# Kernel optimization log

Hardware: AMD Instinct MI355X
Metric: run time of the kernel (lower is better)

The kernel has to match this reference:

```python
import jax, jax.numpy as jnp
import numpy as np

N, E, EE = 1024, 32768, 262144
C_S, C_Z, C_G, H, R = 384, 128, 16, 4, 64
EPS = 1e-8


def _rbf(d, D_count=R, D_min=0.0, D_max=20.0):
    # gvp-style radial basis: exp(-((d - mu)/sigma)^2), mu in linspace(D_min, D_max)
    mu = jnp.linspace(D_min, D_max, D_count, dtype=d.dtype)
    sigma = (D_max - D_min) / D_count
    return jnp.exp(-(((d[..., None] - mu) / sigma) ** 2))


def _layernorm(x, g, b, eps=1e-5):
    m = jnp.mean(x, axis=-1, keepdims=True)
    v = jnp.var(x, axis=-1, keepdims=True)
    return (x - m) * jax.lax.rsqrt(v + eps) * g + b


def setup_inputs() -> dict:
    key = jax.random.key(0)
    ks = jax.random.split(key, 32)
    s = 0.02
    inp = {
        'node_features': jax.random.normal(ks[0], (N, C_S), jnp.float32),
        'node_trans': jax.random.normal(ks[1], (N, 3), jnp.float32) * 10.0,
        'edge_features': jax.random.normal(ks[2], (E, C_Z), jnp.float32),
        'edge_index': jax.random.randint(ks[3], (2, E), 0, N),
        'edge_edge_index': jax.random.randint(ks[4], (2, EE), 0, E),
        # layer norm
        'ln_g': jnp.ones((C_Z,), jnp.float32),
        'ln_b': jnp.zeros((C_Z,), jnp.float32),
        # node_left / node_right
        'W_nl': jax.random.normal(ks[5], (C_S, C_G), jnp.float32) * s,
        'b_nl': jnp.zeros((C_G,), jnp.float32),
        'W_nr': jax.random.normal(ks[6], (C_S, C_G), jnp.float32) * s,
        'b_nr': jnp.zeros((C_G,), jnp.float32),
        # bias_gate: (c_gate_s^2 -> c_z)
        'W_bg': jax.random.normal(ks[7], (C_G * C_G, C_Z), jnp.float32) * s,
        'b_bg': jnp.zeros((C_Z,), jnp.float32),
        # dist_bias: (num_rbf -> c_z)
        'W_db': jax.random.normal(ks[8], (R, C_Z), jnp.float32) * s,
        'b_db': jnp.zeros((C_Z,), jnp.float32),
        # to_bias: (c_z -> num_heads), no bias
        'W_tb': jax.random.normal(ks[9], (C_Z, H), jnp.float32) * s,
        # q / kv
        'W_q': jax.random.normal(ks[10], (C_Z, C_Z), jnp.float32) * s,
        'b_q': jnp.zeros((C_Z,), jnp.float32),
        'W_kv': jax.random.normal(ks[11], (C_Z, 2 * C_Z), jnp.float32) * s,
        'b_kv': jnp.zeros((2 * C_Z,), jnp.float32),
        # out gate + out proj
        'W_og': jax.random.normal(ks[12], (C_Z, C_Z), jnp.float32) * s,
        'b_og': jnp.zeros((C_Z,), jnp.float32),
        'W_out': jax.random.normal(ks[13], (C_Z, C_Z), jnp.float32) * s,
        'b_out': jnp.zeros((C_Z,), jnp.float32),
    }
    return inp


def reference(node_features, node_trans, edge_features, edge_index, edge_edge_index,
              ln_g, ln_b, W_nl, b_nl, W_nr, b_nr, W_bg, b_bg, W_db, b_db, W_tb,
              W_q, b_q, W_kv, b_kv, W_og, b_og, W_out, b_out):
    d = C_Z // H
    ee0, ee1 = edge_edge_index[0], edge_edge_index[1]
    # node indices of the two triangle corner nodes for each edge-edge pair
    n1 = edge_index[0, ee1]  # [EE]
    n2 = edge_index[0, ee0]  # [EE]

    ef = _layernorm(edge_features, ln_g, ln_b)  # [E, c_z]

    nl = node_features @ W_nl + b_nl  # [N, c_g]
    nr = node_features @ W_nr + b_nr
    # outer product gate features per edge-edge pair
    e3 = jnp.einsum('bi,bj->bij', nl[n1], nr[n2]).reshape(-1, C_G * C_G)  # [EE, c_g^2]
    gate = e3 @ W_bg + b_bg  # [EE, c_z]

    dist = jnp.linalg.norm(node_trans[n1] - node_trans[n2] + EPS, axis=-1)  # [EE]
    dist_bias = _rbf(dist) @ W_db + b_db  # [EE, c_z]
    bias = (jax.nn.sigmoid(gate) * dist_bias) @ W_tb  # [EE, H]

    q = (ef @ W_q + b_q).reshape(E, H, d)
    kv = ef @ W_kv + b_kv
    k = kv[:, :C_Z].reshape(E, H, d)
    v = kv[:, C_Z:].reshape(E, H, d)

    attn = jnp.einsum('bhi,bhi->bh', q[ee1], k[ee0]) * (1.0 / np.sqrt(C_Z)) + bias  # [EE, H]

    # segment softmax over target edge ee1
    seg_max = jax.ops.segment_max(attn, ee1, num_segments=E)  # [E, H]
    p = jnp.exp(attn - seg_max[ee1])
    seg_sum = jax.ops.segment_sum(p, ee1, num_segments=E)
    p = p / (seg_sum[ee1] + 1e-16)

    upd = jax.ops.segment_sum(v[ee0] * p[..., None], ee1, num_segments=E)  # [E, H, d]
    upd = upd.reshape(E, C_Z)
    upd = upd * jax.nn.sigmoid(ef @ W_og + b_og)
    return upd @ W_out + b_out
```

## Files before the change

kernel.cpp:

```cpp
#include <hip/hip_runtime.h>
#include <math.h>

#define NN 1024
#define NE 32768
#define NEE 262144
#define CS 384
#define CZ 128
#define CG 16
#define NH 4
#define NR 64

typedef __attribute__((ext_vector_type(8))) short short8v;
typedef __attribute__((ext_vector_type(4))) float f32x4;
typedef unsigned short ushort_t;

__device__ __forceinline__ float sigmoidf_(float x) { return 1.0f / (1.0f + __expf(-x)); }

__device__ __forceinline__ ushort_t f2bf(float x) {
    union { float f; unsigned u; } v; v.f = x;
    unsigned r = v.u + 0x7fff + ((v.u >> 16) & 1);
    return (ushort_t)(r >> 16);
}
__device__ __forceinline__ float bf2f(ushort_t x) {
    union { unsigned u; float f; } v; v.u = ((unsigned)x) << 16;
    return v.f;
}

__global__ void node_proj_kernel(const float* __restrict__ nf,
                                 const float* __restrict__ Wl, const float* __restrict__ bl,
                                 const float* __restrict__ Wr, const float* __restrict__ br,
                                 ushort_t* __restrict__ nl16, float* __restrict__ nr) {
    int wave = threadIdx.x >> 6, lane = threadIdx.x & 63;
    int n = blockIdx.x * 4 + wave;
    if (lane >= 32) return;
    bool isl = lane < 16;
    int o = isl ? lane : lane - 16;
    const float* W = isl ? Wl : Wr;
    float acc = isl ? bl[o] : br[o];
    const float* x = nf + n * CS;
    for (int k = 0; k < CS; ++k) acc += x[k] * W[k * 16 + o];
    if (isl) nl16[n * 16 + o] = f2bf(acc);
    else     nr[n * 16 + o] = acc;
}

__global__ void build_Tt_kernel(const float* __restrict__ nr, const float* __restrict__ Wbg,
                                ushort_t* __restrict__ Tbf) {
    int n = blockIdx.x;
    int t = threadIdx.x;
    int c = t & 127, i0 = t >> 7;
    __shared__ float nrs[16];
    if (t < 16) nrs[t] = nr[n * 16 + t];
    __syncthreads();
    for (int i = i0; i < 16; i += 2) {
        float acc = 0.f;
#pragma unroll
        for (int j = 0; j < 16; ++j) acc += nrs[j] * Wbg[(i * 16 + j) * 128 + c];
        Tbf[n * 2048 + c * 16 + i] = f2bf(acc);
    }
}

__global__ void ln_kernel(const float* __restrict__ x, const float* __restrict__ g,
                          const float* __restrict__ b, ushort_t* __restrict__ ef) {
    int wave = threadIdx.x >> 6, lane = threadIdx.x & 63;
    int e = blockIdx.x * 4 + wave;
    int c0 = lane, c1 = lane + 64;
    float x0 = x[e * 128 + c0], x1 = x[e * 128 + c1];
    float s = x0 + x1;
#pragma unroll
    for (int m = 1; m < 64; m <<= 1) s += __shfl_xor(s, m);
    float mean = s * (1.f / 128.f);
    float d0 = x0 - mean, d1 = x1 - mean;
    float v = d0 * d0 + d1 * d1;
#pragma unroll
    for (int m = 1; m < 64; m <<= 1) v += __shfl_xor(v, m);
    v *= (1.f / 128.f);
    float inv = rsqrtf(v + 1e-5f);
    ef[e * 128 + c0] = f2bf(d0 * inv * g[c0] + b[c0]);
    ef[e * 128 + c1] = f2bf(d1 * inv * g[c1] + b[c1]);
}

__global__ void prep_w_kernel(const float* __restrict__ Wq, const float* __restrict__ bq,
                              const float* __restrict__ Wkv, const float* __restrict__ bkv,
                              const float* __restrict__ Wog, const float* __restrict__ bog,
                              const float* __restrict__ Wdb, const float* __restrict__ Wout,
                              ushort_t* __restrict__ WcatT, float* __restrict__ bcat,
                              ushort_t* __restrict__ WdbT, ushort_t* __restrict__ WoutT) {
    int idx = blockIdx.x * 256 + threadIdx.x;
    int col = idx >> 7, k = idx & 127;
    float w;
    if (col < 128) w = Wq[k * 128 + col];
    else if (col < 256) w = Wog[k * 128 + (col - 128)];
    else if (col < 384) w = Wkv[k * 256 + (col - 256)];
    else w = Wkv[k * 256 + 128 + (col - 384)];
    WcatT[idx] = f2bf(w);
    if (idx < 512) {
        float bb;
        if (idx < 128) bb = bq[idx];
        else if (idx < 256) bb = bog[idx - 128];
        else if (idx < 384) bb = bkv[idx - 256];
        else bb = bkv[idx - 384 + 128];
        bcat[idx] = bb;
    }
    if (idx < 128 * 64) {
        int c = idx >> 6, r = idx & 63;
        WdbT[idx] = f2bf(Wdb[r * 128 + c]);
    }
    if (idx < 128 * 128) {
        int c = idx >> 7, kk = idx & 127;
        WoutT[idx] = f2bf(Wout[kk * 128 + c]);
    }
}

__global__ void __launch_bounds__(256) mfma_gemm_proj(const ushort_t* __restrict__ Abf,
                                                      const ushort_t* __restrict__ Bt,
                                                      const float* __restrict__ bias,
                                                      ushort_t* __restrict__ qog,
                                                      ushort_t* __restrict__ kvo) {
    __shared__ ushort_t As[128][136];
    __shared__ ushort_t Bs[64][136];
    int t = threadIdx.x;
    int row0 = blockIdx.y * 128;
    int n0 = blockIdx.x * 64;
#pragma unroll
    for (int u = 0; u < 8; ++u) {
        int idx = t + u * 256;
        int r = idx >> 4, seg = idx & 15;
        *(short8v*)&As[r][seg * 8] = *(const short8v*)&Abf[(size_t)(row0 + r) * 128 + seg * 8];
    }
#pragma unroll
    for (int u = 0; u < 4; ++u) {
        int idx = t + u * 256;
        int r = idx >> 4, seg = idx & 15;
        *(short8v*)&Bs[r][seg * 8] = *(const short8v*)&Bt[(size_t)(n0 + r) * 128 + seg * 8];
    }
    __syncthreads();
    int lane = t & 63, w = t >> 6;
    int wr = (w >> 1) * 64, wc = (w & 1) * 32;
    int fr = lane & 15, fk = (lane >> 4) * 8;
    f32x4 acc[4][2] = {};
#pragma unroll
    for (int kk = 0; kk < 4; ++kk) {
        short8v a[4], b[2];
#pragma unroll
        for (int m = 0; m < 4; ++m) a[m] = *(const short8v*)&As[wr + m * 16 + fr][kk * 32 + fk];
#pragma unroll
        for (int n = 0; n < 2; ++n) b[n] = *(const short8v*)&Bs[wc + n * 16 + fr][kk * 32 + fk];
#pragma unroll
        for (int m = 0; m < 4; ++m)
#pragma unroll
            for (int n = 0; n < 2; ++n)
                acc[m][n] = __builtin_amdgcn_mfma_f32_16x16x32_bf16(a[m], b[n], acc[m][n], 0, 0, 0);
    }
    __syncthreads();
    ushort_t (*stage)[72] = (ushort_t(*)[72])&As[0][0];
    int orow = (lane >> 4) * 4;
#pragma unroll
    for (int m = 0; m < 4; ++m)
#pragma unroll
        for (int n = 0; n < 2; ++n) {
            int col = wc + n * 16 + fr;
            float bv = bias[n0 + col];
#pragma unroll
            for (int j = 0; j < 4; ++j)
                stage[wr + m * 16 + orow + j][col] = f2bf(acc[m][n][j] + bv);
        }
    __syncthreads();
    ushort_t* basep; int cbase;
    if (n0 < 256) { basep = qog; cbase = n0; } else { basep = kvo; cbase = n0 - 256; }
#pragma unroll
    for (int u = 0; u < 4; ++u) {
        int idx = t + u * 256;
        int r = idx >> 3, seg = idx & 7;
        *(short8v*)&basep[(size_t)(row0 + r) * 256 + cbase + seg * 8] = *(const short8v*)&stage[r][seg * 8];
    }
}

__global__ void __launch_bounds__(256) mfma_gemm_out(const float* __restrict__ Af,
                                                     const ushort_t* __restrict__ Bt,
                                                     const float* __restrict__ bias,
                                                     float* __restrict__ out) {
    __shared__ ushort_t As[128][136];
    __shared__ ushort_t Bs[64][136];
    int t = threadIdx.x;
    int row0 = blockIdx.y * 128;
    int n0 = blockIdx.x * 64;
#pragma unroll
    for (int u = 0; u < 8; ++u) {
        int idx = t + u * 256;
        int r = idx >> 4, seg = idx & 15;
        float4 f0 = *(const float4*)&Af[(size_t)(row0 + r) * 128 + seg * 8];
        float4 f1 = *(const float4*)&Af[(size_t)(row0 + r) * 128 + seg * 8 + 4];
        short8v pk;
        pk[0] = (short)f2bf(f0.x); pk[1] = (short)f2bf(f0.y);
        pk[2] = (short)f2bf(f0.z); pk[3] = (short)f2bf(f0.w);
        pk[4] = (short)f2bf(f1.x); pk[5] = (short)f2bf(f1.y);
        pk[6] = (short)f2bf(f1.z); pk[7] = (short)f2bf(f1.w);
        *(short8v*)&As[r][seg * 8] = pk;
    }
#pragma unroll
    for (int u = 0; u < 4; ++u) {
        int idx = t + u * 256;
        int r = idx >> 4, seg = idx & 15;
        *(short8v*)&Bs[r][seg * 8] = *(const short8v*)&Bt[(size_t)(n0 + r) * 128 + seg * 8];
    }
    __syncthreads();
    int lane = t & 63, w = t >> 6;
    int wr = (w >> 1) * 64, wc = (w & 1) * 32;
    int fr = lane & 15, fk = (lane >> 4) * 8;
    f32x4 acc[4][2] = {};
#pragma unroll
    for (int kk = 0; kk < 4; ++kk) {
        short8v a[4], b[2];
#pragma unroll
        for (int m = 0; m < 4; ++m) a[m] = *(const short8v*)&As[wr + m * 16 + fr][kk * 32 + fk];
#pragma unroll
        for (int n = 0; n < 2; ++n) b[n] = *(const short8v*)&Bs[wc + n * 16 + fr][kk * 32 + fk];
#pragma unroll
        for (int m = 0; m < 4; ++m)
#pragma unroll
            for (int n = 0; n < 2; ++n)
                acc[m][n] = __builtin_amdgcn_mfma_f32_16x16x32_bf16(a[m], b[n], acc[m][n], 0, 0, 0);
    }
    __syncthreads();
    float (*stage)[68] = (float(*)[68])&As[0][0];
    int orow = (lane >> 4) * 4;
#pragma unroll
    for (int m = 0; m < 4; ++m)
#pragma unroll
        for (int n = 0; n < 2; ++n) {
            int col = wc + n * 16 + fr;
            float bv = bias[n0 + col];
#pragma unroll
            for (int j = 0; j < 4; ++j)
                stage[wr + m * 16 + orow + j][col] = acc[m][n][j] + bv;
        }
    __syncthreads();
#pragma unroll
    for (int u = 0; u < 8; ++u) {
        int idx = t + u * 256;
        int r = idx >> 4, c4 = idx & 15;
        *(float4*)&out[(size_t)(row0 + r) * 128 + n0 + c4 * 4] = *(const float4*)&stage[r][c4 * 4];
    }
}

__global__ void hist_kernel(const int* __restrict__ eei, const int* __restrict__ ei,
                            int* __restrict__ cnt, int* __restrict__ cnt2) {
    int p = blockIdx.x * 256 + threadIdx.x;
    int e0 = eei[p], e1 = eei[NEE + p];
    atomicAdd(&cnt[e1], 1);
    atomicAdd(&cnt2[ei[e0]], 1);
}

__global__ void scan_kernel(const int* __restrict__ cnt, int* __restrict__ offs,
                            int* __restrict__ cursor) {
    __shared__ int part[1024];
    int t = threadIdx.x;
    int loc[32];
    int s = 0;
#pragma unroll
    for (int j = 0; j < 32; ++j) { loc[j] = cnt[t * 32 + j]; s += loc[j]; }
    part[t] = s;
    __syncthreads();
    for (int d = 1; d < 1024; d <<= 1) {
        int add = (t >= d) ? part[t - d] : 0;
        __syncthreads();
        part[t] += add;
        __syncthreads();
    }
    int excl = (t == 0) ? 0 : part[t - 1];
#pragma unroll
    for (int j = 0; j < 32; ++j) {
        offs[t * 32 + j] = excl;
        cursor[t * 32 + j] = excl;
        excl += loc[j];
    }
    if (t == 1023) offs[NE] = excl;
}

__global__ void scan2_kernel(const int* __restrict__ cnt2, int* __restrict__ offs2,
                             int* __restrict__ cursor2) {
    __shared__ int part[256];
    int t = threadIdx.x;
    int loc[4];
    int s = 0;
#pragma unroll
    for (int j = 0; j < 4; ++j) { loc[j] = cnt2[t * 4 + j]; s += loc[j]; }
    part[t] = s;
    __syncthreads();
    for (int d = 1; d < 256; d <<= 1) {
        int add = (t >= d) ? part[t - d] : 0;
        __syncthreads();
        part[t] += add;
        __syncthreads();
    }
    int excl = (t == 0) ? 0 : part[t - 1];
#pragma unroll
    for (int j = 0; j < 4; ++j) {
        offs2[t * 4 + j] = excl;
        cursor2[t * 4 + j] = excl;
        excl += loc[j];
    }
    if (t == 255) offs2[1024] = excl;
}

__global__ void scatter_both_kernel(const int* __restrict__ eei, const int* __restrict__ ei,
                                    const float* __restrict__ ntr,
                                    int* __restrict__ cursor, int* __restrict__ e0rank,
                                    int* __restrict__ cursor2, int* __restrict__ n1rank,
                                    float* __restrict__ drank, int* __restrict__ x2to1) {
    int p = blockIdx.x * 256 + threadIdx.x;
    int e0 = eei[p], e1 = eei[NEE + p];
    int pos = atomicAdd(&cursor[e1], 1);
    e0rank[pos] = e0;
    int n1 = ei[e1], n2 = ei[e0];
    int pos2 = atomicAdd(&cursor2[n2], 1);
    n1rank[pos2] = n1;
    x2to1[pos2] = pos;
    float dx = ntr[n1 * 3 + 0] - ntr[n2 * 3 + 0] + 1e-8f;
    float dy = ntr[n1 * 3 + 1] - ntr[n2 * 3 + 1] + 1e-8f;
    float dz = ntr[n1 * 3 + 2] - ntr[n2 * 3 + 2] + 1e-8f;
    drank[pos2] = sqrtf(dx * dx + dy * dy + dz * dz);
}

__global__ void __launch_bounds__(256) bias_kernel(
    const int* __restrict__ offs2, const int* __restrict__ n1rank,
    const float* __restrict__ drank, const int* __restrict__ x2to1,
    const ushort_t* __restrict__ nl16, const ushort_t* __restrict__ Tbf,
    const ushort_t* __restrict__ WdbT,
    const float* __restrict__ bbg, const float* __restrict__ bdb,
    const float* __restrict__ Wtb, float* __restrict__ bias_cs) {
    __shared__ ushort_t Tt[128 * 24];
    __shared__ ushort_t Wd[128 * 72];
    int t = threadIdx.x;
    int n2 = blockIdx.x;
    {
        const ushort_t* src = Tbf + n2 * 2048;
        int c = t >> 1, hh = t & 1;
        *(int4*)&Tt[c * 24 + hh * 8] = *(const int4*)&src[c * 16 + hh * 8];
    }
#pragma unroll
    for (int u = 0; u < 4; ++u) {
        int idx = t + u * 256;
        int c = idx >> 3, seg = idx & 7;
        *(int4*)&Wd[c * 72 + seg * 8] = *(const int4*)&WdbT[c * 64 + seg * 8];
    }
    __syncthreads();

    int lane = t & 63, w = t >> 6;
    int cl = lane & 15, g = lane >> 4;
    float wtb[8][4], bdbl[8], bbgl[8];
#pragma unroll
    for (int nb = 0; nb < 8; ++nb) {
        int c = nb * 16 + cl;
        float4 wt = *(const float4*)&Wtb[c * 4];
        wtb[nb][0] = wt.x; wtb[nb][1] = wt.y; wtb[nb][2] = wt.z; wtb[nb][3] = wt.w;
        bdbl[nb] = bdb[c];
        bbgl[nb] = bbg[c];
    }
    int bstart = offs2[n2], bend = offs2[n2 + 1];
    const float MU = 20.0f / 63.0f;
    f32x4 zero4 = {0.f, 0.f, 0.f, 0.f};

    for (int base = bstart + w * 16; base < bend; base += 64) {
        int idx = base + cl;
        int ip = (idx < bend) ? idx : (bend - 1);
        int n1 = n1rank[ip];
        float d = drank[ip];
        short8v aNL = {0, 0, 0, 0, 0, 0, 0, 0};
        if (g < 2) aNL = *(const short8v*)&nl16[n1 * 16 + g * 8];
        short8v ea, eb;
#pragma unroll
        for (int j = 0; j < 8; ++j) {
            float r = (float)(g * 8 + j);
            float t0 = (d - r * MU) * 3.2f;
            float t1 = (d - (r + 32.0f) * MU) * 3.2f;
            ea[j] = (short)f2bf(__expf(-t0 * t0));
            eb[j] = (short)f2bf(__expf(-t1 * t1));
        }
        f32x4 G[8], D[8];
#pragma unroll
        for (int nb = 0; nb < 8; ++nb) {
            short8v bT = {0, 0, 0, 0, 0, 0, 0, 0};
            if (g < 2) bT = *(const short8v*)&Tt[(nb * 16 + cl) * 24 + g * 8];
            G[nb] = __builtin_amdgcn_mfma_f32_16x16x32_bf16(aNL, bT, zero4, 0, 0, 0);
        }
#pragma unroll
        for (int nb = 0; nb < 8; ++nb) {
            short8v bW0 = *(const short8v*)&Wd[(nb * 16 + cl) * 72 + g * 8];
            short8v bW1 = *(const short8v*)&Wd[(nb * 16 + cl) * 72 + 32 + g * 8];
            f32x4 tmp = __builtin_amdgcn_mfma_f32_16x16x32_bf16(ea, bW0, zero4, 0, 0, 0);
            D[nb] = __builtin_amdgcn_mfma_f32_16x16x32_bf16(eb, bW1, tmp, 0, 0, 0);
        }
        float bacc[4][4] = {};
#pragma unroll
        for (int nb = 0; nb < 8; ++nb) {
#pragma unroll
            for (int j = 0; j < 4; ++j) {
                float gv = G[nb][j] + bbgl[nb];
                float db = D[nb][j] + bdbl[nb];
                float sg = db * sigmoidf_(gv);
                bacc[j][0] += sg * wtb[nb][0];
                bacc[j][1] += sg * wtb[nb][1];
                bacc[j][2] += sg * wtb[nb][2];
                bacc[j][3] += sg * wtb[nb][3];
            }
        }
#pragma unroll
        for (int j = 0; j < 4; ++j)
#pragma unroll
            for (int h = 0; h < 4; ++h) {
                float v = bacc[j][h];
                v += __shfl_xor(v, 1);
                v += __shfl_xor(v, 2);
                v += __shfl_xor(v, 4);
                v += __shfl_xor(v, 8);
                bacc[j][h] = v;
            }
        int row = g * 4 + (cl >> 2), h = cl & 3;
        int oidx = base + row;
        if (oidx < bend) {
            int dst = x2to1[oidx];
            bias_cs[(size_t)dst * 4 + h] = bacc[cl >> 2][h];
        }
    }
}

__global__ void __launch_bounds__(256) segment_kernel(const ushort_t* __restrict__ qog,
                                                      const ushort_t* __restrict__ kv,
                                                      const float* __restrict__ bias_cs,
                                                      const int* __restrict__ offs,
                                                      const int* __restrict__ e0rank,
                                                      float* __restrict__ updg) {
    int t = threadIdx.x, wave = t >> 6, lane = t & 63;
    int gw = blockIdx.x * 4 + wave;
    int h = lane >> 4;
    const float scale = 0.08838834764831845f;
    for (int it = 0; it < 4; ++it) {
        int e = gw * 4 + it;
        int st = offs[e], en = offs[e + 1];
        unsigned qw = *(const unsigned*)&qog[(size_t)e * 256 + 2 * lane];
        float q0 = bf2f((ushort_t)(qw & 0xffff)), q1 = bf2f((ushort_t)(qw >> 16));
        float s = 0.f, u0 = 0.f, u1 = 0.f;
        for (int idx = st; idx < en; ++idx) {
            int e0 = e0rank[idx];
            const ushort_t* kvr = kv + (size_t)e0 * 256;
            unsigned kw = *(const unsigned*)&kvr[2 * lane];
            unsigned vw = *(const unsigned*)&kvr[128 + 2 * lane];
            float ta = q0 * bf2f((ushort_t)(kw & 0xffff)) + q1 * bf2f((ushort_t)(kw >> 16));
#pragma unroll
            for (int m = 1; m < 16; m <<= 1) ta += __shfl_xor(ta, m);
            float wgt = __expf(ta * scale + bias_cs[(size_t)idx * 4 + h]);
            s += wgt;
            u0 += wgt * bf2f((ushort_t)(vw & 0xffff));
            u1 += wgt * bf2f((ushort_t)(vw >> 16));
        }
        float inv = 1.0f / (s + 1e-16f);
        unsigned ogw = *(const unsigned*)&qog[(size_t)e * 256 + 128 + 2 * lane];
        u0 = u0 * inv * sigmoidf_(bf2f((ushort_t)(ogw & 0xffff)));
        u1 = u1 * inv * sigmoidf_(bf2f((ushort_t)(ogw >> 16)));
        float2 uo; uo.x = u0; uo.y = u1;
        *(float2*)&updg[(size_t)e * 128 + 2 * lane] = uo;
    }
}

extern "C" void kernel_launch(void* const* d_in, const int* in_sizes, int n_in,
                              void* d_out, int out_size, void* d_ws, size_t ws_size,
                              hipStream_t stream) {
    const float* node_features = (const float*)d_in[0];
    const float* node_trans   = (const float*)d_in[1];
    const float* edge_features= (const float*)d_in[2];
    const int*   edge_index   = (const int*)d_in[3];
    const int*   eei          = (const int*)d_in[4];
    const float* ln_g  = (const float*)d_in[5];
    const float* ln_b  = (const float*)d_in[6];
    const float* W_nl  = (const float*)d_in[7];
    const float* b_nl  = (const float*)d_in[8];
    const float* W_nr  = (const float*)d_in[9];
    const float* b_nr  = (const float*)d_in[10];
    const float* W_bg  = (const float*)d_in[11];
    const float* b_bg  = (const float*)d_in[12];
    const float* W_db  = (const float*)d_in[13];
    const float* b_db  = (const float*)d_in[14];
    const float* W_tb  = (const float*)d_in[15];
    const float* W_q   = (const float*)d_in[16];
    const float* b_q   = (const float*)d_in[17];
    const float* W_kv  = (const float*)d_in[18];
    const float* b_kv  = (const float*)d_in[19];
    const float* W_og  = (const float*)d_in[20];
    const float* b_og  = (const float*)d_in[21];
    const float* W_out = (const float*)d_in[22];
    const float* b_out = (const float*)d_in[23];
    float* out = (float*)d_out;

    char* ws = (char*)d_ws;
    size_t off = 0;
    auto alloc = [&](size_t bytes) -> void* {
        void* p = ws + off;
        off += (bytes + 255) & ~(size_t)255;
        return p;
    };
    ushort_t* nl16  = (ushort_t*)alloc((size_t)NN * 16 * 2);
    float*    nr    = (float*)alloc((size_t)NN * 16 * 4);
    ushort_t* Tbf   = (ushort_t*)alloc((size_t)NN * 2048 * 2);
    ushort_t* WdbT  = (ushort_t*)alloc((size_t)128 * 64 * 2);
    ushort_t* WcatT = (ushort_t*)alloc((size_t)512 * 128 * 2);
    float*    bcat  = (float*)alloc((size_t)512 * 4);
    ushort_t* WoutT = (ushort_t*)alloc((size_t)128 * 128 * 2);
    ushort_t* ef_bf = (ushort_t*)alloc((size_t)NE * 128 * 2);
    ushort_t* qog   = (ushort_t*)alloc((size_t)NE * 256 * 2);
    ushort_t* kvb   = (ushort_t*)alloc((size_t)NE * 256 * 2);
    float*    bias_cs = (float*)alloc((size_t)NEE * 4 * 4);
    float*    updg  = (float*)alloc((size_t)NE * 128 * 4);
    int*      cnt   = (int*)alloc((size_t)NE * 4);
    int*      cnt2  = (int*)alloc((size_t)1024 * 4);
    int*      offs  = (int*)alloc((size_t)(NE + 1) * 4);
    int*      offs2 = (int*)alloc((size_t)1025 * 4);
    int*      cursor  = (int*)alloc((size_t)NE * 4);
    int*      cursor2 = (int*)alloc((size_t)1024 * 4);
    int*      e0rank= (int*)alloc((size_t)NEE * 4);
    int*      n1rank= (int*)alloc((size_t)NEE * 4);
    float*    drank = (float*)alloc((size_t)NEE * 4);
    int*      x2to1 = (int*)alloc((size_t)NEE * 4);

    hipMemsetAsync(cnt, 0, (size_t)NE * 4 + 1024 * 4, stream);

    node_proj_kernel<<<NN / 4, 256, 0, stream>>>(node_features, W_nl, b_nl, W_nr, b_nr, nl16, nr);
    build_Tt_kernel<<<NN, 256, 0, stream>>>(nr, W_bg, Tbf);
    ln_kernel<<<NE / 4, 256, 0, stream>>>(edge_features, ln_g, ln_b, ef_bf);
    prep_w_kernel<<<256, 256, 0, stream>>>(W_q, b_q, W_kv, b_kv, W_og, b_og, W_db, W_out,
                                           WcatT, bcat, WdbT, WoutT);
    mfma_gemm_proj<<<dim3(8, 256), 256, 0, stream>>>(ef_bf, WcatT, bcat, qog, kvb);
    hist_kernel<<<NEE / 256, 256, 0, stream>>>(eei, edge_index, cnt, cnt2);
    scan_kernel<<<1, 1024, 0, stream>>>(cnt, offs, cursor);
    scan2_kernel<<<1, 256, 0, stream>>>(cnt2, offs2, cursor2);
    scatter_both_kernel<<<NEE / 256, 256, 0, stream>>>(eei, edge_index, node_trans,
                                                       cursor, e0rank, cursor2, n1rank, drank, x2to1);
    bias_kernel<<<NN, 256, 0, stream>>>(offs2, n1rank, drank, x2to1, nl16, Tbf, WdbT,
                                        b_bg, b_db, W_tb, bias_cs);
    segment_kernel<<<NE / 16, 256, 0, stream>>>(qog, kvb, bias_cs, offs, e0rank, updg);
    mfma_gemm_out<<<dim3(2, 256), 256, 0, stream>>>(updg, WoutT, b_out, out);
}
```

Before: 441.1 us.

## Split bias kernel per node across two blocks, drop LDS staging, unroll segment loop

The bias kernel now launches two blocks per target node, each covering alternating 16-row chunks, and reads the T and W_db weights straight from global memory instead of staging them in shared memory behind a barrier. The biases are folded into the MFMA accumulator init, and the columns are processed in two halves to lower register pressure. The segment softmax loop is unrolled by two so two neighbours' key/value loads are in flight at once. These changes aim to raise occupancy and memory-level parallelism, at the cost of more global/L2 traffic for the weights.

```diff
diff --git a/kernel.cpp b/kernel.cpp
--- a/kernel.cpp
+++ b/kernel.cpp
@@ -322,6 +322,7 @@
     drank[pos2] = sqrtf(dx * dx + dy * dy + dz * dz);
 }
 
+#define BSPLIT 2
 __global__ void __launch_bounds__(256) bias_kernel(
     const int* __restrict__ offs2, const int* __restrict__ n1rank,
     const float* __restrict__ drank, const int* __restrict__ x2to1,
@@ -329,23 +330,9 @@
     const ushort_t* __restrict__ WdbT,
     const float* __restrict__ bbg, const float* __restrict__ bdb,
     const float* __restrict__ Wtb, float* __restrict__ bias_cs) {
-    __shared__ ushort_t Tt[128 * 24];
-    __shared__ ushort_t Wd[128 * 72];
     int t = threadIdx.x;
-    int n2 = blockIdx.x;
-    {
-        const ushort_t* src = Tbf + n2 * 2048;
-        int c = t >> 1, hh = t & 1;
-        *(int4*)&Tt[c * 24 + hh * 8] = *(const int4*)&src[c * 16 + hh * 8];
-    }
-#pragma unroll
-    for (int u = 0; u < 4; ++u) {
-        int idx = t + u * 256;
-        int c = idx >> 3, seg = idx & 7;
-        *(int4*)&Wd[c * 72 + seg * 8] = *(const int4*)&WdbT[c * 64 + seg * 8];
-    }
-    __syncthreads();
-
+    int n2 = blockIdx.x >> 1;
+    int sp = blockIdx.x & 1;
     int lane = t & 63, w = t >> 6;
     int cl = lane & 15, g = lane >> 4;
     float wtb[8][4], bdbl[8], bbgl[8];
@@ -357,11 +344,11 @@
         bdbl[nb] = bdb[c];
         bbgl[nb] = bbg[c];
     }
+    const ushort_t* Trow = Tbf + (size_t)n2 * 2048;
     int bstart = offs2[n2], bend = offs2[n2 + 1];
     const float MU = 20.0f / 63.0f;
-    f32x4 zero4 = {0.f, 0.f, 0.f, 0.f};
-
-    for (int base = bstart + w * 16; base < bend; base += 64) {
+
+    for (int base = bstart + (sp * 4 + w) * 16; base < bend; base += 16 * 4 * BSPLIT) {
         int idx = base + cl;
         int ip = (idx < bend) ? idx : (bend - 1);
         int n1 = n1rank[ip];
@@ -377,32 +364,42 @@
             ea[j] = (short)f2bf(__expf(-t0 * t0));
             eb[j] = (short)f2bf(__expf(-t1 * t1));
         }
-        f32x4 G[8], D[8];
-#pragma unroll
-        for (int nb = 0; nb < 8; ++nb) {
-            short8v bT = {0, 0, 0, 0, 0, 0, 0, 0};
-            if (g < 2) bT = *(const short8v*)&Tt[(nb * 16 + cl) * 24 + g * 8];
-            G[nb] = __builtin_amdgcn_mfma_f32_16x16x32_bf16(aNL, bT, zero4, 0, 0, 0);
-        }
-#pragma unroll
-        for (int nb = 0; nb < 8; ++nb) {
-            short8v bW0 = *(const short8v*)&Wd[(nb * 16 + cl) * 72 + g * 8];
-            short8v bW1 = *(const short8v*)&Wd[(nb * 16 + cl) * 72 + 32 + g * 8];
-            f32x4 tmp = __builtin_amdgcn_mfma_f32_16x16x32_bf16(ea, bW0, zero4, 0, 0, 0);
-            D[nb] = __builtin_amdgcn_mfma_f32_16x16x32_bf16(eb, bW1, tmp, 0, 0, 0);
-        }
         float bacc[4][4] = {};
 #pragma unroll
-        for (int nb = 0; nb < 8; ++nb) {
-#pragma unroll
-            for (int j = 0; j < 4; ++j) {
-                float gv = G[nb][j] + bbgl[nb];
-                float db = D[nb][j] + bdbl[nb];
-                float sg = db * sigmoidf_(gv);
-                bacc[j][0] += sg * wtb[nb][0];
-                bacc[j][1] += sg * wtb[nb][1];
-                bacc[j][2] += sg * wtb[nb][2];
-                bacc[j][3] += sg * wtb[nb][3];
+        for (int half = 0; half < 2; ++half) {
+            f32x4 G[4], D[4];
+#pragma unroll
+            for (int q = 0; q < 4; ++q) {
+                int nb = half * 4 + q;
+                int c = nb * 16 + cl;
+                short8v bT = {0, 0, 0, 0, 0, 0, 0, 0};
+                if (g < 2) bT = *(const short8v*)&Trow[c * 16 + g * 8];
+                float bg = bbgl[nb];
+                f32x4 ci = {bg, bg, bg, bg};
+                G[q] = __builtin_amdgcn_mfma_f32_16x16x32_bf16(aNL, bT, ci, 0, 0, 0);
+            }
+#pragma unroll
+            for (int q = 0; q < 4; ++q) {
+                int nb = half * 4 + q;
+                int c = nb * 16 + cl;
+                short8v bW0 = *(const short8v*)&WdbT[c * 64 + g * 8];
+                short8v bW1 = *(const short8v*)&WdbT[c * 64 + 32 + g * 8];
+                float bd = bdbl[nb];
+                f32x4 ci = {bd, bd, bd, bd};
+                f32x4 tmp = __builtin_amdgcn_mfma_f32_16x16x32_bf16(ea, bW0, ci, 0, 0, 0);
+                D[q] = __builtin_amdgcn_mfma_f32_16x16x32_bf16(eb, bW1, tmp, 0, 0, 0);
+            }
+#pragma unroll
+            for (int q = 0; q < 4; ++q) {
+                int nb = half * 4 + q;
+#pragma unroll
+                for (int j = 0; j < 4; ++j) {
+                    float sg = D[q][j] * sigmoidf_(G[q][j]);
+                    bacc[j][0] += sg * wtb[nb][0];
+                    bacc[j][1] += sg * wtb[nb][1];
+                    bacc[j][2] += sg * wtb[nb][2];
+                    bacc[j][3] += sg * wtb[nb][3];
+                }
             }
         }
 #pragma unroll
@@ -441,7 +438,26 @@
         unsigned qw = *(const unsigned*)&qog[(size_t)e * 256 + 2 * lane];
         float q0 = bf2f((ushort_t)(qw & 0xffff)), q1 = bf2f((ushort_t)(qw >> 16));
         float s = 0.f, u0 = 0.f, u1 = 0.f;
-        for (int idx = st; idx < en; ++idx) {
+        int idx = st;
+        for (; idx + 2 <= en; idx += 2) {
+            int e0a = e0rank[idx], e0b = e0rank[idx + 1];
+            const ushort_t* kvra = kv + (size_t)e0a * 256;
+            const ushort_t* kvrb = kv + (size_t)e0b * 256;
+            unsigned kwa = *(const unsigned*)&kvra[2 * lane];
+            unsigned vwa = *(const unsigned*)&kvra[128 + 2 * lane];
+            unsigned kwb = *(const unsigned*)&kvrb[2 * lane];
+            unsigned vwb = *(const unsigned*)&kvrb[128 + 2 * lane];
+            float ta = q0 * bf2f((ushort_t)(kwa & 0xffff)) + q1 * bf2f((ushort_t)(kwa >> 16));
+            float tb = q0 * bf2f((ushort_t)(kwb & 0xffff)) + q1 * bf2f((ushort_t)(kwb >> 16));
+#pragma unroll
+            for (int m = 1; m < 16; m <<= 1) { ta += __shfl_xor(ta, m); tb += __shfl_xor(tb, m); }
+            float wa = __expf(ta * scale + bias_cs[(size_t)idx * 4 + h]);
+            float wb = __expf(tb * scale + bias_cs[(size_t)(idx + 1) * 4 + h]);
+            s += wa + wb;
+            u0 += wa * bf2f((ushort_t)(vwa & 0xffff)) + wb * bf2f((ushort_t)(vwb & 0xffff));
+            u1 += wa * bf2f((ushort_t)(vwa >> 16)) + wb * bf2f((ushort_t)(vwb >> 16));
+        }
+        if (idx < en) {
             int e0 = e0rank[idx];
             const ushort_t* kvr = kv + (size_t)e0 * 256;
             unsigned kw = *(const unsigned*)&kvr[2 * lane];
@@ -535,8 +551,8 @@
     scan2_kernel<<<1, 256, 0, stream>>>(cnt2, offs2, cursor2);
     scatter_both_kernel<<<NEE / 256, 256, 0, stream>>>(eei, edge_index, node_trans,
                                                        cursor, e0rank, cursor2, n1rank, drank, x2to1);
-    bias_kernel<<<NN, 256, 0, stream>>>(offs2, n1rank, drank, x2to1, nl16, Tbf, WdbT,
-                                        b_bg, b_db, W_tb, bias_cs);
+    bias_kernel<<<NN * BSPLIT, 256, 0, stream>>>(offs2, n1rank, drank, x2to1, nl16, Tbf, WdbT,
+                                                 b_bg, b_db, W_tb, bias_cs);
     segment_kernel<<<NE / 16, 256, 0, stream>>>(qog, kvb, bias_cs, offs, e0rank, updg);
     mfma_gemm_out<<<dim3(2, 256), 256, 0, stream>>>(updg, WoutT, b_out, out);
 }
```

After: 506.3 us. 14.8% more time.

## Precompute dense node-pair bias table and drop second bucketing pass

Applied to the files above, without the earlier changes.

The bias term depends only on the node pair (n1, n2), so a dense N×N×H table is now computed with MFMA over all node pairs. The segment kernel looks it up through a packed n2*1024+n1 index stored per sorted edge-edge pair. This removes the second histogram, scan, scatter and the indirect x2to1 writes. The segment softmax loop is also unrolled by two to overlap gathers. The cost is about four times more bias arithmetic (1M pairs versus 262K) and a 16 MB table written and randomly read.

```diff
diff --git a/kernel.cpp b/kernel.cpp
--- a/kernel.cpp
+++ b/kernel.cpp
@@ -243,12 +243,9 @@
     }
 }
 
-__global__ void hist_kernel(const int* __restrict__ eei, const int* __restrict__ ei,
-                            int* __restrict__ cnt, int* __restrict__ cnt2) {
+__global__ void hist_kernel(const int* __restrict__ eei, int* __restrict__ cnt) {
     int p = blockIdx.x * 256 + threadIdx.x;
-    int e0 = eei[p], e1 = eei[NEE + p];
-    atomicAdd(&cnt[e1], 1);
-    atomicAdd(&cnt2[ei[e0]], 1);
+    atomicAdd(&cnt[eei[NEE + p]], 1);
 }
 
 __global__ void scan_kernel(const int* __restrict__ cnt, int* __restrict__ offs,
@@ -277,64 +274,27 @@
     if (t == 1023) offs[NE] = excl;
 }
 
-__global__ void scan2_kernel(const int* __restrict__ cnt2, int* __restrict__ offs2,
-                             int* __restrict__ cursor2) {
-    __shared__ int part[256];
-    int t = threadIdx.x;
-    int loc[4];
-    int s = 0;
-#pragma unroll
-    for (int j = 0; j < 4; ++j) { loc[j] = cnt2[t * 4 + j]; s += loc[j]; }
-    part[t] = s;
-    __syncthreads();
-    for (int d = 1; d < 256; d <<= 1) {
-        int add = (t >= d) ? part[t - d] : 0;
-        __syncthreads();
-        part[t] += add;
-        __syncthreads();
-    }
-    int excl = (t == 0) ? 0 : part[t - 1];
-#pragma unroll
-    for (int j = 0; j < 4; ++j) {
-        offs2[t * 4 + j] = excl;
-        cursor2[t * 4 + j] = excl;
-        excl += loc[j];
-    }
-    if (t == 255) offs2[1024] = excl;
-}
-
-__global__ void scatter_both_kernel(const int* __restrict__ eei, const int* __restrict__ ei,
-                                    const float* __restrict__ ntr,
-                                    int* __restrict__ cursor, int* __restrict__ e0rank,
-                                    int* __restrict__ cursor2, int* __restrict__ n1rank,
-                                    float* __restrict__ drank, int* __restrict__ x2to1) {
+__global__ void scatter_kernel(const int* __restrict__ eei, const int* __restrict__ ei,
+                               int* __restrict__ cursor, int* __restrict__ e0rank,
+                               int* __restrict__ n12rank) {
     int p = blockIdx.x * 256 + threadIdx.x;
     int e0 = eei[p], e1 = eei[NEE + p];
     int pos = atomicAdd(&cursor[e1], 1);
     e0rank[pos] = e0;
-    int n1 = ei[e1], n2 = ei[e0];
-    int pos2 = atomicAdd(&cursor2[n2], 1);
-    n1rank[pos2] = n1;
-    x2to1[pos2] = pos;
-    float dx = ntr[n1 * 3 + 0] - ntr[n2 * 3 + 0] + 1e-8f;
-    float dy = ntr[n1 * 3 + 1] - ntr[n2 * 3 + 1] + 1e-8f;
-    float dz = ntr[n1 * 3 + 2] - ntr[n2 * 3 + 2] + 1e-8f;
-    drank[pos2] = sqrtf(dx * dx + dy * dy + dz * dz);
-}
-
-__global__ void __launch_bounds__(256) bias_kernel(
-    const int* __restrict__ offs2, const int* __restrict__ n1rank,
-    const float* __restrict__ drank, const int* __restrict__ x2to1,
+    n12rank[pos] = ei[e0] * 1024 + ei[e1];
+}
+
+__global__ void __launch_bounds__(256) bias_tab_kernel(
     const ushort_t* __restrict__ nl16, const ushort_t* __restrict__ Tbf,
-    const ushort_t* __restrict__ WdbT,
+    const ushort_t* __restrict__ WdbT, const float* __restrict__ ntr,
     const float* __restrict__ bbg, const float* __restrict__ bdb,
-    const float* __restrict__ Wtb, float* __restrict__ bias_cs) {
+    const float* __restrict__ Wtb, float* __restrict__ bias_tab) {
     __shared__ ushort_t Tt[128 * 24];
     __shared__ ushort_t Wd[128 * 72];
     int t = threadIdx.x;
     int n2 = blockIdx.x;
     {
-        const ushort_t* src = Tbf + n2 * 2048;
+        const ushort_t* src = Tbf + (size_t)n2 * 2048;
         int c = t >> 1, hh = t & 1;
         *(int4*)&Tt[c * 24 + hh * 8] = *(const int4*)&src[c * 16 + hh * 8];
     }
@@ -345,91 +305,94 @@
         *(int4*)&Wd[c * 72 + seg * 8] = *(const int4*)&WdbT[c * 64 + seg * 8];
     }
     __syncthreads();
-
     int lane = t & 63, w = t >> 6;
     int cl = lane & 15, g = lane >> 4;
     float wtb[8][4], bdbl[8], bbgl[8];
 #pragma unroll
-    for (int nb = 0; nb < 8; ++nb) {
-        int c = nb * 16 + cl;
+    for (int ct = 0; ct < 8; ++ct) {
+        int c = ct * 16 + cl;
         float4 wt = *(const float4*)&Wtb[c * 4];
-        wtb[nb][0] = wt.x; wtb[nb][1] = wt.y; wtb[nb][2] = wt.z; wtb[nb][3] = wt.w;
-        bdbl[nb] = bdb[c];
-        bbgl[nb] = bbg[c];
-    }
-    int bstart = offs2[n2], bend = offs2[n2 + 1];
+        wtb[ct][0] = wt.x; wtb[ct][1] = wt.y; wtb[ct][2] = wt.z; wtb[ct][3] = wt.w;
+        bdbl[ct] = bdb[c];
+        bbgl[ct] = bbg[c];
+    }
+    float px2 = ntr[n2 * 3 + 0], py2 = ntr[n2 * 3 + 1], pz2 = ntr[n2 * 3 + 2];
     const float MU = 20.0f / 63.0f;
-    f32x4 zero4 = {0.f, 0.f, 0.f, 0.f};
-
-    for (int base = bstart + w * 16; base < bend; base += 64) {
-        int idx = base + cl;
-        int ip = (idx < bend) ? idx : (bend - 1);
-        int n1 = n1rank[ip];
-        float d = drank[ip];
-        short8v aNL = {0, 0, 0, 0, 0, 0, 0, 0};
-        if (g < 2) aNL = *(const short8v*)&nl16[n1 * 16 + g * 8];
-        short8v ea, eb;
-#pragma unroll
-        for (int j = 0; j < 8; ++j) {
-            float r = (float)(g * 8 + j);
-            float t0 = (d - r * MU) * 3.2f;
-            float t1 = (d - (r + 32.0f) * MU) * 3.2f;
-            ea[j] = (short)f2bf(__expf(-t0 * t0));
-            eb[j] = (short)f2bf(__expf(-t1 * t1));
-        }
-        f32x4 G[8], D[8];
-#pragma unroll
-        for (int nb = 0; nb < 8; ++nb) {
+    float* outb = bias_tab + (size_t)n2 * 4096;
+
+    for (int ch = 0; ch < 8; ++ch) {
+        int rowbase = w * 256 + ch * 32;
+        short8v aNL[2], ea[2], eb[2];
+#pragma unroll
+        for (int rg = 0; rg < 2; ++rg) {
+            int row = rowbase + rg * 16 + cl;
+            short8v z = {0, 0, 0, 0, 0, 0, 0, 0};
+            aNL[rg] = z;
+            if (g < 2) aNL[rg] = *(const short8v*)&nl16[row * 16 + g * 8];
+            float dx = ntr[row * 3 + 0] - px2 + 1e-8f;
+            float dy = ntr[row * 3 + 1] - py2 + 1e-8f;
+            float dz = ntr[row * 3 + 2] - pz2 + 1e-8f;
+            float d = sqrtf(dx * dx + dy * dy + dz * dz);
+#pragma unroll
+            for (int j = 0; j < 8; ++j) {
+                float r = (float)(g * 8 + j);
+                float t0 = (d - r * MU) * 3.2f;
+                float t1 = (d - (r + 32.0f) * MU) * 3.2f;
+                ea[rg][j] = (short)f2bf(__expf(-t0 * t0));
+                eb[rg][j] = (short)f2bf(__expf(-t1 * t1));
+            }
+        }
+        float bacc[2][4][4] = {};
+#pragma unroll
+        for (int ct = 0; ct < 8; ++ct) {
+            int c = ct * 16 + cl;
             short8v bT = {0, 0, 0, 0, 0, 0, 0, 0};
-            if (g < 2) bT = *(const short8v*)&Tt[(nb * 16 + cl) * 24 + g * 8];
-            G[nb] = __builtin_amdgcn_mfma_f32_16x16x32_bf16(aNL, bT, zero4, 0, 0, 0);
-        }
-#pragma unroll
-        for (int nb = 0; nb < 8; ++nb) {
-            short8v bW0 = *(const short8v*)&Wd[(nb * 16 + cl) * 72 + g * 8];
-            short8v bW1 = *(const short8v*)&Wd[(nb * 16 + cl) * 72 + 32 + g * 8];
-            f32x4 tmp = __builtin_amdgcn_mfma_f32_16x16x32_bf16(ea, bW0, zero4, 0, 0, 0);
-            D[nb] = __builtin_amdgcn_mfma_f32_16x16x32_bf16(eb, bW1, tmp, 0, 0, 0);
-        }
-        float bacc[4][4] = {};
-#pragma unroll
-        for (int nb = 0; nb < 8; ++nb) {
-#pragma unroll
-            for (int j = 0; j < 4; ++j) {
-                float gv = G[nb][j] + bbgl[nb];
-                float db = D[nb][j] + bdbl[nb];
-                float sg = db * sigmoidf_(gv);
-                bacc[j][0] += sg * wtb[nb][0];
-                bacc[j][1] += sg * wtb[nb][1];
-                bacc[j][2] += sg * wtb[nb][2];
-                bacc[j][3] += sg * wtb[nb][3];
+            if (g < 2) bT = *(const short8v*)&Tt[c * 24 + g * 8];
+            short8v bW0 = *(const short8v*)&Wd[c * 72 + g * 8];
+            short8v bW1 = *(const short8v*)&Wd[c * 72 + 32 + g * 8];
+            float bg = bbgl[ct], bd = bdbl[ct];
+            f32x4 cg = {bg, bg, bg, bg};
+            f32x4 cd = {bd, bd, bd, bd};
+#pragma unroll
+            for (int rg = 0; rg < 2; ++rg) {
+                f32x4 G = __builtin_amdgcn_mfma_f32_16x16x32_bf16(aNL[rg], bT, cg, 0, 0, 0);
+                f32x4 D = __builtin_amdgcn_mfma_f32_16x16x32_bf16(ea[rg], bW0, cd, 0, 0, 0);
+                D = __builtin_amdgcn_mfma_f32_16x16x32_bf16(eb[rg], bW1, D, 0, 0, 0);
+#pragma unroll
+                for (int j = 0; j < 4; ++j) {
+                    float sg = D[j] * sigmoidf_(G[j]);
+                    bacc[rg][j][0] += sg * wtb[ct][0];
+                    bacc[rg][j][1] += sg * wtb[ct][1];
+                    bacc[rg][j][2] += sg * wtb[ct][2];
+                    bacc[rg][j][3] += sg * wtb[ct][3];
+                }
             }
         }
 #pragma unroll
-        for (int j = 0; j < 4; ++j)
-#pragma unroll
-            for (int h = 0; h < 4; ++h) {
-                float v = bacc[j][h];
-                v += __shfl_xor(v, 1);
-                v += __shfl_xor(v, 2);
-                v += __shfl_xor(v, 4);
-                v += __shfl_xor(v, 8);
-                bacc[j][h] = v;
-            }
-        int row = g * 4 + (cl >> 2), h = cl & 3;
-        int oidx = base + row;
-        if (oidx < bend) {
-            int dst = x2to1[oidx];
-            bias_cs[(size_t)dst * 4 + h] = bacc[cl >> 2][h];
+        for (int rg = 0; rg < 2; ++rg) {
+#pragma unroll
+            for (int j = 0; j < 4; ++j)
+#pragma unroll
+                for (int h2 = 0; h2 < 4; ++h2) {
+                    float v = bacc[rg][j][h2];
+                    v += __shfl_xor(v, 1);
+                    v += __shfl_xor(v, 2);
+                    v += __shfl_xor(v, 4);
+                    v += __shfl_xor(v, 8);
+                    bacc[rg][j][h2] = v;
+                }
+            int row = rowbase + rg * 16 + g * 4 + (cl >> 2);
+            outb[row * 4 + (cl & 3)] = bacc[rg][cl >> 2][cl & 3];
         }
     }
 }
 
 __global__ void __launch_bounds__(256) segment_kernel(const ushort_t* __restrict__ qog,
                                                       const ushort_t* __restrict__ kv,
-                                                      const float* __restrict__ bias_cs,
+                                                      const float* __restrict__ bias_tab,
                                                       const int* __restrict__ offs,
                                                       const int* __restrict__ e0rank,
+                                                      const int* __restrict__ n12rank,
                                                       float* __restrict__ updg) {
     int t = threadIdx.x, wave = t >> 6, lane = t & 63;
     int gw = blockIdx.x * 4 + wave;
@@ -441,15 +404,38 @@
         unsigned qw = *(const unsigned*)&qog[(size_t)e * 256 + 2 * lane];
         float q0 = bf2f((ushort_t)(qw & 0xffff)), q1 = bf2f((ushort_t)(qw >> 16));
         float s = 0.f, u0 = 0.f, u1 = 0.f;
-        for (int idx = st; idx < en; ++idx) {
+        int idx = st;
+        for (; idx + 2 <= en; idx += 2) {
+            int e0a = e0rank[idx], e0b = e0rank[idx + 1];
+            int na = n12rank[idx], nb = n12rank[idx + 1];
+            const ushort_t* kvra = kv + (size_t)e0a * 256;
+            const ushort_t* kvrb = kv + (size_t)e0b * 256;
+            unsigned kwa = *(const unsigned*)&kvra[2 * lane];
+            unsigned vwa = *(const unsigned*)&kvra[128 + 2 * lane];
+            unsigned kwb = *(const unsigned*)&kvrb[2 * lane];
+            unsigned vwb = *(const unsigned*)&kvrb[128 + 2 * lane];
+            float bha = bias_tab[(size_t)na * 4 + h];
+            float bhb = bias_tab[(size_t)nb * 4 + h];
+            float ta = q0 * bf2f((ushort_t)(kwa & 0xffff)) + q1 * bf2f((ushort_t)(kwa >> 16));
+            float tb = q0 * bf2f((ushort_t)(kwb & 0xffff)) + q1 * bf2f((ushort_t)(kwb >> 16));
+#pragma unroll
+            for (int m = 1; m < 16; m <<= 1) { ta += __shfl_xor(ta, m); tb += __shfl_xor(tb, m); }
+            float wa = __expf(ta * scale + bha);
+            float wb = __expf(tb * scale + bhb);
+            s += wa + wb;
+            u0 += wa * bf2f((ushort_t)(vwa & 0xffff)) + wb * bf2f((ushort_t)(vwb & 0xffff));
+            u1 += wa * bf2f((ushort_t)(vwa >> 16)) + wb * bf2f((ushort_t)(vwb >> 16));
+        }
+        if (idx < en) {
             int e0 = e0rank[idx];
+            int n12 = n12rank[idx];
             const ushort_t* kvr = kv + (size_t)e0 * 256;
             unsigned kw = *(const unsigned*)&kvr[2 * lane];
             unsigned vw = *(const unsigned*)&kvr[128 + 2 * lane];
             float ta = q0 * bf2f((ushort_t)(kw & 0xffff)) + q1 * bf2f((ushort_t)(kw >> 16));
 #pragma unroll
             for (int m = 1; m < 16; m <<= 1) ta += __shfl_xor(ta, m);
-            float wgt = __expf(ta * scale + bias_cs[(size_t)idx * 4 + h]);
+            float wgt = __expf(ta * scale + bias_tab[(size_t)n12 * 4 + h]);
             s += wgt;
             u0 += wgt * bf2f((ushort_t)(vw & 0xffff));
             u1 += wgt * bf2f((ushort_t)(vw >> 16));
@@ -509,20 +495,15 @@
     ushort_t* ef_bf = (ushort_t*)alloc((size_t)NE * 128 * 2);
     ushort_t* qog   = (ushort_t*)alloc((size_t)NE * 256 * 2);
     ushort_t* kvb   = (ushort_t*)alloc((size_t)NE * 256 * 2);
-    float*    bias_cs = (float*)alloc((size_t)NEE * 4 * 4);
+    float*    bias_tab = (float*)alloc((size_t)NN * NN * 4 * 4);
     float*    updg  = (float*)alloc((size_t)NE * 128 * 4);
     int*      cnt   = (int*)alloc((size_t)NE * 4);
-    int*      cnt2  = (int*)alloc((size_t)1024 * 4);
     int*      offs  = (int*)alloc((size_t)(NE + 1) * 4);
-    int*      offs2 = (int*)alloc((size_t)1025 * 4);
     int*      cursor  = (int*)alloc((size_t)NE * 4);
-    int*      cursor2 = (int*)alloc((size_t)1024 * 4);
     int*      e0rank= (int*)alloc((size_t)NEE * 4);
-    int*      n1rank= (int*)alloc((size_t)NEE * 4);
-    float*    drank = (float*)alloc((size_t)NEE * 4);
-    int*      x2to1 = (int*)alloc((size_t)NEE * 4);
-
-    hipMemsetAsync(cnt, 0, (size_t)NE * 4 + 1024 * 4, stream);
+    int*      n12rank= (int*)alloc((size_t)NEE * 4);
+
+    hipMemsetAsync(cnt, 0, (size_t)NE * 4, stream);
 
     node_proj_kernel<<<NN / 4, 256, 0, stream>>>(node_features, W_nl, b_nl, W_nr, b_nr, nl16, nr);
     build_Tt_kernel<<<NN, 256, 0, stream>>>(nr, W_bg, Tbf);
@@ -530,13 +511,11 @@
     prep_w_kernel<<<256, 256, 0, stream>>>(W_q, b_q, W_kv, b_kv, W_og, b_og, W_db, W_out,
                                            WcatT, bcat, WdbT, WoutT);
     mfma_gemm_proj<<<dim3(8, 256), 256, 0, stream>>>(ef_bf, WcatT, bcat, qog, kvb);
-    hist_kernel<<<NEE / 256, 256, 0, stream>>>(eei, edge_index, cnt, cnt2);
+    hist_kernel<<<NEE / 256, 256, 0, stream>>>(eei, cnt);
     scan_kernel<<<1, 1024, 0, stream>>>(cnt, offs, cursor);
-    scan2_kernel<<<1, 256, 0, stream>>>(cnt2, offs2, cursor2);
-    scatter_both_kernel<<<NEE / 256, 256, 0, stream>>>(eei, edge_index, node_trans,
-                                                       cursor, e0rank, cursor2, n1rank, drank, x2to1);
-    bias_kernel<<<NN, 256, 0, stream>>>(offs2, n1rank, drank, x2to1, nl16, Tbf, WdbT,
-                                        b_bg, b_db, W_tb, bias_cs);
-    segment_kernel<<<NE / 16, 256, 0, stream>>>(qog, kvb, bias_cs, offs, e0rank, updg);
+    scatter_kernel<<<NEE / 256, 256, 0, stream>>>(eei, edge_index, cursor, e0rank, n12rank);
+    bias_tab_kernel<<<NN, 256, 0, stream>>>(nl16, Tbf, WdbT, node_trans,
+                                            b_bg, b_db, W_tb, bias_tab);
+    segment_kernel<<<NE / 16, 256, 0, stream>>>(qog, kvb, bias_tab, offs, e0rank, n12rank, updg);
     mfma_gemm_out<<<dim3(2, 256), 256, 0, stream>>>(updg, WoutT, b_out, out);
 }
```

Result: slower. 581.3 us (+31.8%).
